# Kernel optimization log

Measured on AMD Instinct MI355X. Metric: run time of the kernel, lower is better.

The kernel has to match this reference:

```python
import jax, jax.numpy as jnp
import numpy as np

N = 50000          # nodes
E = 1600000        # edges (avg degree 32)
IN = 256
OUT = 16
HEADS = 8
NEG_SLOPE = 0.2


def setup_inputs() -> dict:
    key = jax.random.key(0)
    k1, k2, k3, k4, k5, k6 = jax.random.split(key, 6)
    row = jax.random.randint(k1, (E,), 0, N)            # destination node of each edge
    col = jax.random.randint(k2, (E,), 0, N)            # source node of each edge
    h = jax.random.normal(k3, (N, IN), dtype=jnp.float32)
    # xavier-uniform-like scales
    w_scale = float(np.sqrt(6.0 / (IN + OUT * HEADS)))
    a_scale = float(np.sqrt(6.0 / (HEADS * OUT + 1)))
    W = jax.random.uniform(k4, (IN, OUT * HEADS), jnp.float32, -w_scale, w_scale)
    a_l = jax.random.uniform(k5, (1, HEADS, OUT), jnp.float32, -a_scale, a_scale)
    a_r = jax.random.uniform(k6, (1, HEADS, OUT), jnp.float32, -a_scale, a_scale)
    return {"row": row, "col": col, "h": h, "W": W, "a_l": a_l, "a_r": a_r}


def reference(row, col, h, W, a_l, a_r):
    n = h.shape[0]
    heads, out = a_l.shape[1], a_l.shape[2]
    Wh = (h @ W).reshape(n, heads, out)                 # [N, H, D]
    Wh1 = (Wh * a_l).sum(2)                             # [N, H]
    Wh2 = (Wh * a_r).sum(2)                             # [N, H]
    e = Wh1[row] + Wh2[col]                             # [E, H]
    e = jnp.where(e > 0, e, NEG_SLOPE * e)              # leaky relu
    # segment (row-wise) softmax over edges sharing the same destination row
    m = jax.ops.segment_max(e, row, num_segments=n)     # [N, H]
    ex = jnp.exp(e - m[row])                            # [E, H]
    s = jax.ops.segment_sum(ex, row, num_segments=n)    # [N, H]
    alpha = ex / s[row]                                 # [E, H]
    # torch .reshape(-1, out, heads) reinterprets memory layout (NOT a transpose)
    Wh_r = Wh.reshape(n, out, heads)                    # [N, D, H]
    msg = alpha[:, None, :] * Wh_r[col]                 # [E, D, H]
    h_prime = jax.ops.segment_sum(msg, row, num_segments=n)  # [N, D, H]
    return jax.nn.relu(h_prime)
```

## Files before the change

### kernel.cpp

```cpp
#include <hip/hip_runtime.h>
#include <cfloat>
#include <math.h>


constexpr int IN_F  = 256;
constexpr int F     = 128;
constexpr int HEADS = 8;
constexpr int BS    = 32;
constexpr int BSH   = 5;
constexpr int SLAB  = 2048;
constexpr int CSLAB = 9216;
constexpr int PTILE = 4096;

typedef __attribute__((ext_vector_type(8))) short bf16x8;
typedef __attribute__((ext_vector_type(4))) float f32x4;

__device__ inline uint f2bf(float x) {
    uint u = __float_as_uint(x);
    return (u + 0x7fffu + ((u >> 16) & 1u)) >> 16;
}
__device__ inline uint pack2(float a, float b) { return f2bf(a) | (f2bf(b) << 16); }

__global__ __launch_bounds__(256) void prepack(const float* __restrict__ W,
                                               uint4* __restrict__ Wf,
                                               int* __restrict__ cursorC,
                                               int* __restrict__ cursorF,
                                               int NC, int NBF)
{
    if (blockIdx.x == 0) {
        for (int i = threadIdx.x; i < NC; i += 256) cursorC[i] = i * CSLAB;
        for (int i = threadIdx.x; i < NBF; i += 256) cursorF[i] = i * SLAB;
    }
    int t = blockIdx.x * 256 + threadIdx.x;
    if (t >= 8 * 8 * 64) return;
    int ks = t >> 9, nt = (t >> 6) & 7, l = t & 63;
    int col = nt * 16 + (l & 15);
    int k0 = ks * 32 + (l >> 4) * 8;
    float v[8];
#pragma unroll
    for (int i = 0; i < 8; ++i) v[i] = W[(size_t)(k0 + i) * F + col];
    Wf[t] = make_uint4(pack2(v[0], v[1]), pack2(v[2], v[3]),
                       pack2(v[4], v[5]), pack2(v[6], v[7]));
}

__global__ __launch_bounds__(256) void gemm_wh(
    const float* __restrict__ h, const uint4* __restrict__ Wf,
    const float* __restrict__ a_l, const float* __restrict__ a_r,
    uint* __restrict__ Whb, float* __restrict__ Wh1, float* __restrict__ Wh2, int n)
{
    const int tid = threadIdx.x;
    const int w = tid >> 6, l = tid & 63;
    const int r0 = blockIdx.x * 64 + w * 16;
    const int rA = min(r0 + (l & 15), n - 1);
    const int kb = (l >> 4) * 8;

    const float* hp = &h[(size_t)rA * IN_F + kb];
    f32x4 af[16];
#pragma unroll
    for (int ks = 0; ks < 8; ++ks) {
        af[2 * ks]     = __builtin_nontemporal_load((const f32x4*)(hp + ks * 32));
        af[2 * ks + 1] = __builtin_nontemporal_load((const f32x4*)(hp + ks * 32 + 4));
    }
    uint4 Abf[8];
#pragma unroll
    for (int ks = 0; ks < 8; ++ks) {
        f32x4 a0 = af[2 * ks], a1 = af[2 * ks + 1];
        Abf[ks] = make_uint4(pack2(a0[0], a0[1]), pack2(a0[2], a0[3]),
                             pack2(a1[0], a1[1]), pack2(a1[2], a1[3]));
    }

    f32x4 acc[8];
#pragma unroll
    for (int i = 0; i < 8; ++i) acc[i] = (f32x4)0.f;

#pragma unroll
    for (int ks = 0; ks < 8; ++ks) {
        union { uint4 u; bf16x8 v; } A;
        A.u = Abf[ks];
        const uint4* wp = &Wf[ks * 512 + l];
#pragma unroll
        for (int nt = 0; nt < 8; ++nt) {
            union { uint4 u; bf16x8 v; } B;
            B.u = wp[nt * 64];
            acc[nt] = __builtin_amdgcn_mfma_f32_16x16x32_bf16(A.v, B.v, acc[nt], 0, 0, 0);
        }
    }

    const int c16 = l & 15;
    const int rowm = r0 + 4 * (l >> 4);
    float al[8], ar[8];
#pragma unroll
    for (int H = 0; H < 8; ++H) {
        al[H] = a_l[H * 16 + c16];
        ar[H] = a_r[H * 16 + c16];
    }
#pragma unroll
    for (int reg = 0; reg < 4; ++reg) {
        const int r = rowm + reg;
        float s1v[8], s2v[8];
#pragma unroll
        for (int H = 0; H < 8; ++H) {
            float wv = acc[H][reg];
            s1v[H] = wv * al[H];
            s2v[H] = wv * ar[H];
        }
#pragma unroll
        for (int d = 1; d <= 8; d <<= 1) {
#pragma unroll
            for (int H = 0; H < 8; ++H) {
                s1v[H] += __shfl_xor(s1v[H], d);
                s2v[H] += __shfl_xor(s2v[H], d);
            }
        }
        if (r < n) {
#pragma unroll
            for (int nt = 0; nt < 4; ++nt)
                Whb[(size_t)r * 64 + nt * 16 + c16] = pack2(acc[nt][reg], acc[nt + 4][reg]);
            if (c16 == 0) {
                *(float4*)&Wh1[r * 8]     = make_float4(s1v[0], s1v[1], s1v[2], s1v[3]);
                *(float4*)&Wh1[r * 8 + 4] = make_float4(s1v[4], s1v[5], s1v[6], s1v[7]);
                *(float4*)&Wh2[r * 8]     = make_float4(s2v[0], s2v[1], s2v[2], s2v[3]);
                *(float4*)&Wh2[r * 8 + 4] = make_float4(s2v[4], s2v[5], s2v[6], s2v[7]);
            }
        }
    }
}

__global__ __launch_bounds__(256) void push1_kernel(
    const int* __restrict__ row, const int* __restrict__ col,
    int* __restrict__ cursorC, uint* __restrict__ cpairs, int E)
{
    __shared__ uint stage[PTILE];
    __shared__ int hist[256], st[256], cur[256], gbase[256];
    const int t = threadIdx.x;
    const int i0 = blockIdx.x * PTILE;
    const int cnt = min(PTILE, E - i0);
    hist[t] = 0;
    __syncthreads();

    uint u[PTILE / 256];
#pragma unroll
    for (int j = 0; j < PTILE / 256; ++j) {
        const int idx = t + j * 256;
        if (idx < cnt) {
            int r = row[i0 + idx], c = col[i0 + idx];
            u[j] = ((uint)(r >> 8) << 24) | ((uint)c << 8) | (uint)(r & 255);
            atomicAdd(&hist[r >> 8], 1);
        } else u[j] = 0xFFFFFFFFu;
    }
    __syncthreads();

    const int v = hist[t];
    st[t] = v;
    __syncthreads();
    for (int off = 1; off < 256; off <<= 1) {
        int x = (t >= off) ? st[t - off] : 0;
        __syncthreads();
        st[t] += x;
        __syncthreads();
    }
    cur[t] = st[t] - v;
    if (v) gbase[t] = atomicAdd(&cursorC[t], v);
    __syncthreads();

#pragma unroll
    for (int j = 0; j < PTILE / 256; ++j) {
        if (u[j] != 0xFFFFFFFFu) {
            int k = u[j] >> 24;
            int pos = atomicAdd(&cur[k], 1);
            stage[pos] = u[j];
        }
    }
    __syncthreads();

    for (int p = t; p < cnt; p += 256) {
        uint wv = stage[p];
        int k = wv >> 24;
        int lstart = st[k] - hist[k];
        __builtin_nontemporal_store(wv & 0xFFFFFFu, &cpairs[gbase[k] + (p - lstart)]);
    }
}

__global__ __launch_bounds__(256) void push2_kernel(
    const uint* __restrict__ cpairs, const int* __restrict__ cursorC,
    int* __restrict__ cursorF, uint* __restrict__ pairs)
{
    __shared__ int hl[8];
    __shared__ int cur8[8];
    const int c = blockIdx.x;
    const int p0 = c * CSLAB;
    const int ec = cursorC[c] - p0;
    const int t = threadIdx.x;
    if (t < 8) hl[t] = 0;
    __syncthreads();
    for (int p = t; p < ec; p += 256)
        atomicAdd(&hl[(cpairs[p0 + p] >> 5) & 7], 1);
    __syncthreads();
    if (t < 8)
        cur8[t] = hl[t] ? atomicAdd(&cursorF[c * 8 + t], hl[t]) : 0;
    __syncthreads();
    for (int p = t; p < ec; p += 256) {
        uint u = cpairs[p0 + p];
        int pos = atomicAdd(&cur8[(u >> 5) & 7], 1);
        __builtin_nontemporal_store(((u >> 8) << 5) | (u & 31), &pairs[pos]);
    }
}

__global__ __launch_bounds__(256) void bucket_gat(
    const uint* __restrict__ pairs, const int* __restrict__ cursorF,
    const uint* __restrict__ Whb, const float* __restrict__ Wh1,
    const float* __restrict__ Wh2, float* __restrict__ out, int n)
{
    __shared__ uint cols_l[SLAB];
    __shared__ int cnt_l[BS], st0[BS], cur_l[BS];
    const int t = threadIdx.x;
    const int b = blockIdx.x;
    const int p0 = b * SLAB;
    const int ec = cursorF[b] - p0;

    if (t < BS) cnt_l[t] = 0;
    __syncthreads();
    for (int p = t; p < ec; p += 256)
        atomicAdd(&cnt_l[pairs[p0 + p] & (BS - 1)], 1);
    __syncthreads();
    if (t < BS) {
        int v = cnt_l[t];
        int inc = v;
#pragma unroll
        for (int off = 1; off < BS; off <<= 1) {
            int x = __shfl_up(inc, off);
            if (t >= off) inc += x;
        }
        st0[t] = inc - v;
        cur_l[t] = inc - v;
    }
    __syncthreads();
    for (int p = t; p < ec; p += 256) {
        uint u = pairs[p0 + p];
        int slot = atomicAdd(&cur_l[u & (BS - 1)], 1);
        cols_l[slot] = u >> BSH;
    }
    __syncthreads();

    const int wv = t >> 6, lane = t & 63;
    const int h8 = lane & 7, es = lane >> 3;
#pragma unroll 1
    for (int i = 0; i < 8; ++i) {
        const int rl = wv * 8 + i;
        const int r = (b << BSH) + rl;
        if (r >= n) continue;
        const float w1 = Wh1[r * HEADS + h8];
        const int st = st0[rl];
        const int deg = cnt_l[rl];

        float acc0 = 0.f, acc1 = 0.f, sm = 0.f;
        for (int g = 0; g < deg; g += 8) {
            const int kk = g + es;
            const bool valid = kk < deg;
            const uint c = cols_l[st + (valid ? kk : deg - 1)];
            float e = w1 + Wh2[c * HEADS + h8];
            e = e > 0.f ? e : 0.2f * e;
            e = fminf(e, 60.f);
            const float ex = valid ? __expf(e) : 0.f;
            sm += ex;
            const int m8 = deg - g;
            if (m8 >= 8) {
#pragma unroll
                for (int k = 0; k < 8; ++k) {
                    float pA = __shfl(ex, k * 8 + h8);
                    uint ck = cols_l[st + g + k];
                    uint wb = Whb[((size_t)ck << 6) + lane];
                    acc0 = fmaf(pA, __uint_as_float(wb << 16), acc0);
                    acc1 = fmaf(pA, __uint_as_float(wb & 0xffff0000u), acc1);
                }
            } else {
                for (int k = 0; k < m8; ++k) {
                    float pA = __shfl(ex, k * 8 + h8);
                    uint ck = cols_l[st + g + k];
                    uint wb = Whb[((size_t)ck << 6) + lane];
                    acc0 = fmaf(pA, __uint_as_float(wb << 16), acc0);
                    acc1 = fmaf(pA, __uint_as_float(wb & 0xffff0000u), acc1);
                }
            }
        }
        sm += __shfl_xor(sm, 8);
        sm += __shfl_xor(sm, 16);
        sm += __shfl_xor(sm, 32);
        const float inv = (deg > 0) ? 1.f / sm : 0.f;
        __builtin_nontemporal_store(fmaxf(acc0 * inv, 0.f), &out[(size_t)r * F + lane]);
        __builtin_nontemporal_store(fmaxf(acc1 * inv, 0.f), &out[(size_t)r * F + 64 + lane]);
    }
}

extern "C" void kernel_launch(void* const* d_in, const int* in_sizes, int n_in,
                              void* d_out, int out_size, void* d_ws, size_t ws_size,
                              hipStream_t stream)
{
    const int* row = (const int*)d_in[0];
    const int* col = (const int*)d_in[1];
    const float* h   = (const float*)d_in[2];
    const float* W   = (const float*)d_in[3];
    const float* a_l = (const float*)d_in[4];
    const float* a_r = (const float*)d_in[5];
    const int E = in_sizes[0];
    const int n = in_sizes[2] / IN_F;
    float* out = (float*)d_out;
    const int NBF = (n + BS - 1) >> BSH;
    const int NC  = (n + 255) >> 8;

    char* p = (char*)d_ws;
    auto alloc = [&](size_t bytes) -> char* {
        char* q = p;
        p += (bytes + 255) & ~(size_t)255;
        return q;
    };
    uint*  Whb     = (uint*)alloc((size_t)n * 64 * 4);
    float* Wh1     = (float*)alloc((size_t)n * HEADS * 4);
    float* Wh2     = (float*)alloc((size_t)n * HEADS * 4);
    uint4* Wf      = (uint4*)alloc(8 * 8 * 64 * 16);
    int*   cursorC = (int*)alloc((size_t)NC * 4);
    int*   cursorF = (int*)alloc((size_t)NBF * 4);
    uint*  cpairs  = (uint*)alloc((size_t)NC * CSLAB * 4);
    uint*  pairs   = (uint*)alloc((size_t)NBF * SLAB * 4);

    prepack<<<16, 256, 0, stream>>>(W, Wf, cursorC, cursorF, NC, NBF);
    gemm_wh<<<(n + 63) / 64, 256, 0, stream>>>(h, Wf, a_l, a_r, Whb, Wh1, Wh2, n);
    push1_kernel<<<(E + PTILE - 1) / PTILE, 256, 0, stream>>>(row, col, cursorC, cpairs, E);
    push2_kernel<<<NC, 256, 0, stream>>>(cpairs, cursorC, cursorF, pairs);
    bucket_gat<<<NBF, 256, 0, stream>>>(pairs, cursorF, Whb, Wh1, Wh2, out, n);
}
```

Measured before the change: 150.1 us.

## Merge GEMM and edge bucketing into one launch; process two rows per wave

The GEMM and the first edge-bucketing pass now run as one kernel whose blocks branch on block index. The two independent phases can overlap on the GPU and one launch boundary disappears. The aggregation loop also handles two destination rows per wavefront at once, which doubles the gather loads in flight to hide memory latency. The cost is that GEMM blocks now reserve the push phase's shared memory, which may lower occupancy, plus more registers and divergent handling when the two rows have different degrees.

```diff
diff --git a/kernel.cpp b/kernel.cpp
--- a/kernel.cpp
+++ b/kernel.cpp
@@ -43,12 +43,69 @@
                        pack2(v[4], v[5]), pack2(v[6], v[7]));
 }
 
-__global__ __launch_bounds__(256) void gemm_wh(
+__global__ __launch_bounds__(256) void gemm_push(
     const float* __restrict__ h, const uint4* __restrict__ Wf,
     const float* __restrict__ a_l, const float* __restrict__ a_r,
-    uint* __restrict__ Whb, float* __restrict__ Wh1, float* __restrict__ Wh2, int n)
-{
+    uint* __restrict__ Whb, float* __restrict__ Wh1, float* __restrict__ Wh2,
+    int n, int NGEMM,
+    const int* __restrict__ row, const int* __restrict__ col,
+    int* __restrict__ cursorC, uint* __restrict__ cpairs, int E)
+{
+    __shared__ uint stage[PTILE];
+    __shared__ int hist[256], st[256], cur[256], gbase[256];
     const int tid = threadIdx.x;
+
+    if (blockIdx.x >= NGEMM) {
+        const int t = tid;
+        const int i0 = (blockIdx.x - NGEMM) * PTILE;
+        const int cnt = min(PTILE, E - i0);
+        hist[t] = 0;
+        __syncthreads();
+
+        uint u[PTILE / 256];
+#pragma unroll
+        for (int j = 0; j < PTILE / 256; ++j) {
+            const int idx = t + j * 256;
+            if (idx < cnt) {
+                int r = row[i0 + idx], c = col[i0 + idx];
+                u[j] = ((uint)(r >> 8) << 24) | ((uint)c << 8) | (uint)(r & 255);
+                atomicAdd(&hist[r >> 8], 1);
+            } else u[j] = 0xFFFFFFFFu;
+        }
+        __syncthreads();
+
+        const int v = hist[t];
+        st[t] = v;
+        __syncthreads();
+        for (int off = 1; off < 256; off <<= 1) {
+            int x = (t >= off) ? st[t - off] : 0;
+            __syncthreads();
+            st[t] += x;
+            __syncthreads();
+        }
+        cur[t] = st[t] - v;
+        if (v) gbase[t] = atomicAdd(&cursorC[t], v);
+        __syncthreads();
+
+#pragma unroll
+        for (int j = 0; j < PTILE / 256; ++j) {
+            if (u[j] != 0xFFFFFFFFu) {
+                int k = u[j] >> 24;
+                int pos = atomicAdd(&cur[k], 1);
+                stage[pos] = u[j];
+            }
+        }
+        __syncthreads();
+
+        for (int p = t; p < cnt; p += 256) {
+            uint wv = stage[p];
+            int k = wv >> 24;
+            int lstart = st[k] - hist[k];
+            __builtin_nontemporal_store(wv & 0xFFFFFFu, &cpairs[gbase[k] + (p - lstart)]);
+        }
+        return;
+    }
+
     const int w = tid >> 6, l = tid & 63;
     const int r0 = blockIdx.x * 64 + w * 16;
     const int rA = min(r0 + (l & 15), n - 1);
@@ -126,61 +183,6 @@
     }
 }
 
-__global__ __launch_bounds__(256) void push1_kernel(
-    const int* __restrict__ row, const int* __restrict__ col,
-    int* __restrict__ cursorC, uint* __restrict__ cpairs, int E)
-{
-    __shared__ uint stage[PTILE];
-    __shared__ int hist[256], st[256], cur[256], gbase[256];
-    const int t = threadIdx.x;
-    const int i0 = blockIdx.x * PTILE;
-    const int cnt = min(PTILE, E - i0);
-    hist[t] = 0;
-    __syncthreads();
-
-    uint u[PTILE / 256];
-#pragma unroll
-    for (int j = 0; j < PTILE / 256; ++j) {
-        const int idx = t + j * 256;
-        if (idx < cnt) {
-            int r = row[i0 + idx], c = col[i0 + idx];
-            u[j] = ((uint)(r >> 8) << 24) | ((uint)c << 8) | (uint)(r & 255);
-            atomicAdd(&hist[r >> 8], 1);
-        } else u[j] = 0xFFFFFFFFu;
-    }
-    __syncthreads();
-
-    const int v = hist[t];
-    st[t] = v;
-    __syncthreads();
-    for (int off = 1; off < 256; off <<= 1) {
-        int x = (t >= off) ? st[t - off] : 0;
-        __syncthreads();
-        st[t] += x;
-        __syncthreads();
-    }
-    cur[t] = st[t] - v;
-    if (v) gbase[t] = atomicAdd(&cursorC[t], v);
-    __syncthreads();
-
-#pragma unroll
-    for (int j = 0; j < PTILE / 256; ++j) {
-        if (u[j] != 0xFFFFFFFFu) {
-            int k = u[j] >> 24;
-            int pos = atomicAdd(&cur[k], 1);
-            stage[pos] = u[j];
-        }
-    }
-    __syncthreads();
-
-    for (int p = t; p < cnt; p += 256) {
-        uint wv = stage[p];
-        int k = wv >> 24;
-        int lstart = st[k] - hist[k];
-        __builtin_nontemporal_store(wv & 0xFFFFFFu, &cpairs[gbase[k] + (p - lstart)]);
-    }
-}
-
 __global__ __launch_bounds__(256) void push2_kernel(
     const uint* __restrict__ cpairs, const int* __restrict__ cursorC,
     int* __restrict__ cursorF, uint* __restrict__ pairs)
@@ -245,50 +247,88 @@
     const int wv = t >> 6, lane = t & 63;
     const int h8 = lane & 7, es = lane >> 3;
 #pragma unroll 1
-    for (int i = 0; i < 8; ++i) {
-        const int rl = wv * 8 + i;
-        const int r = (b << BSH) + rl;
-        if (r >= n) continue;
-        const float w1 = Wh1[r * HEADS + h8];
-        const int st = st0[rl];
-        const int deg = cnt_l[rl];
-
-        float acc0 = 0.f, acc1 = 0.f, sm = 0.f;
-        for (int g = 0; g < deg; g += 8) {
-            const int kk = g + es;
-            const bool valid = kk < deg;
-            const uint c = cols_l[st + (valid ? kk : deg - 1)];
-            float e = w1 + Wh2[c * HEADS + h8];
-            e = e > 0.f ? e : 0.2f * e;
-            e = fminf(e, 60.f);
-            const float ex = valid ? __expf(e) : 0.f;
-            sm += ex;
-            const int m8 = deg - g;
-            if (m8 >= 8) {
+    for (int ii = 0; ii < 4; ++ii) {
+        const int rl0 = wv * 8 + 2 * ii;
+        const int rg0 = (b << BSH) + rl0;
+        const int rg1 = rg0 + 1;
+        const bool v0 = rg0 < n, v1 = rg1 < n;
+        const float w1a = v0 ? Wh1[rg0 * HEADS + h8] : 0.f;
+        const float w1b = v1 ? Wh1[rg1 * HEADS + h8] : 0.f;
+        const int stA = st0[rl0], dA = v0 ? cnt_l[rl0] : 0;
+        const int stB = st0[rl0 + 1], dB = v1 ? cnt_l[rl0 + 1] : 0;
+
+        float acc0A = 0.f, acc1A = 0.f, smA = 0.f;
+        float acc0B = 0.f, acc1B = 0.f, smB = 0.f;
+        const int gmax = max(dA, dB);
+        for (int g = 0; g < gmax; g += 8) {
+            float exA = 0.f, exB = 0.f;
+            if (g < dA) {
+                const int kk = g + es;
+                const bool valid = kk < dA;
+                const uint c = cols_l[stA + (valid ? kk : dA - 1)];
+                float e = w1a + Wh2[c * HEADS + h8];
+                e = e > 0.f ? e : 0.2f * e;
+                e = fminf(e, 60.f);
+                exA = valid ? __expf(e) : 0.f;
+                smA += exA;
+            }
+            if (g < dB) {
+                const int kk = g + es;
+                const bool valid = kk < dB;
+                const uint c = cols_l[stB + (valid ? kk : dB - 1)];
+                float e = w1b + Wh2[c * HEADS + h8];
+                e = e > 0.f ? e : 0.2f * e;
+                e = fminf(e, 60.f);
+                exB = valid ? __expf(e) : 0.f;
+                smB += exB;
+            }
+            const int mA = dA - g, mB = dB - g;
+            if (mA >= 8 && mB >= 8) {
 #pragma unroll
                 for (int k = 0; k < 8; ++k) {
-                    float pA = __shfl(ex, k * 8 + h8);
-                    uint ck = cols_l[st + g + k];
-                    uint wb = Whb[((size_t)ck << 6) + lane];
-                    acc0 = fmaf(pA, __uint_as_float(wb << 16), acc0);
-                    acc1 = fmaf(pA, __uint_as_float(wb & 0xffff0000u), acc1);
+                    float pA = __shfl(exA, k * 8 + h8);
+                    float pB = __shfl(exB, k * 8 + h8);
+                    uint ckA = cols_l[stA + g + k];
+                    uint ckB = cols_l[stB + g + k];
+                    uint wbA = Whb[((size_t)ckA << 6) + lane];
+                    uint wbB = Whb[((size_t)ckB << 6) + lane];
+                    acc0A = fmaf(pA, __uint_as_float(wbA << 16), acc0A);
+                    acc1A = fmaf(pA, __uint_as_float(wbA & 0xffff0000u), acc1A);
+                    acc0B = fmaf(pB, __uint_as_float(wbB << 16), acc0B);
+                    acc1B = fmaf(pB, __uint_as_float(wbB & 0xffff0000u), acc1B);
                 }
             } else {
-                for (int k = 0; k < m8; ++k) {
-                    float pA = __shfl(ex, k * 8 + h8);
-                    uint ck = cols_l[st + g + k];
-                    uint wb = Whb[((size_t)ck << 6) + lane];
-                    acc0 = fmaf(pA, __uint_as_float(wb << 16), acc0);
-                    acc1 = fmaf(pA, __uint_as_float(wb & 0xffff0000u), acc1);
+#pragma unroll
+                for (int k = 0; k < 8; ++k) {
+                    if (k < mA) {
+                        float pA = __shfl(exA, k * 8 + h8);
+                        uint ck = cols_l[stA + g + k];
+                        uint wb = Whb[((size_t)ck << 6) + lane];
+                        acc0A = fmaf(pA, __uint_as_float(wb << 16), acc0A);
+                        acc1A = fmaf(pA, __uint_as_float(wb & 0xffff0000u), acc1A);
+                    }
+                    if (k < mB) {
+                        float pB = __shfl(exB, k * 8 + h8);
+                        uint ck = cols_l[stB + g + k];
+                        uint wb = Whb[((size_t)ck << 6) + lane];
+                        acc0B = fmaf(pB, __uint_as_float(wb << 16), acc0B);
+                        acc1B = fmaf(pB, __uint_as_float(wb & 0xffff0000u), acc1B);
+                    }
                 }
             }
         }
-        sm += __shfl_xor(sm, 8);
-        sm += __shfl_xor(sm, 16);
-        sm += __shfl_xor(sm, 32);
-        const float inv = (deg > 0) ? 1.f / sm : 0.f;
-        __builtin_nontemporal_store(fmaxf(acc0 * inv, 0.f), &out[(size_t)r * F + lane]);
-        __builtin_nontemporal_store(fmaxf(acc1 * inv, 0.f), &out[(size_t)r * F + 64 + lane]);
+        smA += __shfl_xor(smA, 8); smA += __shfl_xor(smA, 16); smA += __shfl_xor(smA, 32);
+        smB += __shfl_xor(smB, 8); smB += __shfl_xor(smB, 16); smB += __shfl_xor(smB, 32);
+        if (v0) {
+            const float inv = (dA > 0) ? 1.f / smA : 0.f;
+            __builtin_nontemporal_store(fmaxf(acc0A * inv, 0.f), &out[(size_t)rg0 * F + lane]);
+            __builtin_nontemporal_store(fmaxf(acc1A * inv, 0.f), &out[(size_t)rg0 * F + 64 + lane]);
+        }
+        if (v1) {
+            const float inv = (dB > 0) ? 1.f / smB : 0.f;
+            __builtin_nontemporal_store(fmaxf(acc0B * inv, 0.f), &out[(size_t)rg1 * F + lane]);
+            __builtin_nontemporal_store(fmaxf(acc1B * inv, 0.f), &out[(size_t)rg1 * F + 64 + lane]);
+        }
     }
 }
 
@@ -307,6 +347,8 @@
     float* out = (float*)d_out;
     const int NBF = (n + BS - 1) >> BSH;
     const int NC  = (n + 255) >> 8;
+    const int NGEMM = (n + 63) / 64;
+    const int NPUSH = (E + PTILE - 1) / PTILE;
 
     char* p = (char*)d_ws;
     auto alloc = [&](size_t bytes) -> char* {
@@ -324,8 +366,8 @@
     uint*  pairs   = (uint*)alloc((size_t)NBF * SLAB * 4);
 
     prepack<<<16, 256, 0, stream>>>(W, Wf, cursorC, cursorF, NC, NBF);
-    gemm_wh<<<(n + 63) / 64, 256, 0, stream>>>(h, Wf, a_l, a_r, Whb, Wh1, Wh2, n);
-    push1_kernel<<<(E + PTILE - 1) / PTILE, 256, 0, stream>>>(row, col, cursorC, cpairs, E);
+    gemm_push<<<NGEMM + NPUSH, 256, 0, stream>>>(h, Wf, a_l, a_r, Whb, Wh1, Wh2,
+                                                 n, NGEMM, row, col, cursorC, cpairs, E);
     push2_kernel<<<NC, 256, 0, stream>>>(cpairs, cursorC, cursorF, pairs);
     bucket_gat<<<NBF, 256, 0, stream>>>(pairs, cursorF, Whb, Wh1, Wh2, out, n);
 }
```

Result: slower. 175.5 us (+16.9%).
